# Kernel optimization log

Hardware: AMD Instinct MI355X
Metric: run time of the kernel (lower is better)

The kernel has to match this reference:

```python
import jax, jax.numpy as jnp
import numpy as np

N_NODES = 100000
N_EDGES = 3200000
FEAT = 64  # pos(32) + vel(32)
OUT_DIM = 2


def setup_inputs() -> dict:
    key = jax.random.key(0)
    k1, k2, k3, k4, k5, k6, k7, k8 = jax.random.split(key, 8)
    pos = jax.random.normal(k1, (N_NODES, 32), dtype=jnp.float32)
    vel = jax.random.normal(k2, (N_NODES, 32), dtype=jnp.float32)
    edge_index = jax.random.randint(k3, (2, N_EDGES), 0, N_NODES, dtype=jnp.int64 if jax.config.jax_enable_x64 else jnp.int32)
    s = 1.0 / np.sqrt(FEAT)
    W_rel = jax.random.uniform(k4, (FEAT, FEAT), jnp.float32, -s, s)
    b_rel = jax.random.uniform(k5, (FEAT,), jnp.float32, -s, s)
    W_root = jax.random.uniform(k6, (FEAT, FEAT), jnp.float32, -s, s)
    W_pred = jax.random.uniform(k7, (FEAT, OUT_DIM), jnp.float32, -s, s)
    b_pred = jax.random.uniform(k8, (OUT_DIM,), jnp.float32, -s, s)
    return {"pos": pos, "vel": vel, "edge_index": edge_index,
            "W_rel": W_rel, "b_rel": b_rel, "W_root": W_root,
            "W_pred": W_pred, "b_pred": b_pred}


def reference(pos, vel, edge_index, W_rel, b_rel, W_root, W_pred, b_pred):
    # h = cat([pos, vel], -1)  -> [N, 64]
    h = jnp.concatenate([pos, vel], axis=-1)
    src, dst = edge_index[0], edge_index[1]
    # GraphConv (PyG, aggr='add'): out_i = lin_rel(sum_{j->i} h_j) + lin_root(h_i)
    msgs = h[src]  # [E, 64] irregular gather
    agg = jax.ops.segment_sum(msgs, dst, num_segments=N_NODES)  # [N, 64]
    conv_out = agg @ W_rel + b_rel + h @ W_root
    # lin_pred
    return conv_out @ W_pred + b_pred
```

## Files before the change

kernel.cpp:

```cpp
#include <hip/hip_runtime.h>

#define N_NODES 100000
#define N_EDGES 3200000
#define FEAT 64
#define OUT_DIM 2

#define SHIFT 8
#define S_NODES 256
#define K_BUCKETS 391
#define CAP 8704
#define NB 400
#define EPB (N_EDGES / NB)
#define BT 1024


__global__ __launch_bounds__(256) void node_kernel(const float* __restrict__ pos,
                                                   const float* __restrict__ vel,
                                                   const float* __restrict__ W_rel,
                                                   const float* __restrict__ b_rel,
                                                   const float* __restrict__ W_root,
                                                   const float* __restrict__ W_pred,
                                                   const float* __restrict__ b_pred,
                                                   float* __restrict__ y,
                                                   float* __restrict__ out,
                                                   int* __restrict__ gcount) {
    __shared__ float sM[258];
    int t = threadIdx.x;

    if (blockIdx.x == 0)
        for (int i = t; i < K_BUCKETS; i += 256) gcount[i] = 0;

    {
        const float* W = (t < 128) ? W_rel : W_root;
        int k = (t & 127) >> 1, o = t & 1;
        float acc = 0.f;
        #pragma unroll
        for (int f = 0; f < FEAT; ++f) acc += W[k * FEAT + f] * W_pred[f * OUT_DIM + o];
        sM[t] = acc;
        if (t < OUT_DIM) {
            float b = b_pred[t];
            #pragma unroll
            for (int f = 0; f < FEAT; ++f) b += b_rel[f] * W_pred[f * OUT_DIM + t];
            sM[256 + t] = b;
        }
    }
    __syncthreads();

    int n = blockIdx.x * 256 + t;
    if (n >= N_NODES) return;

    const float4* p4 = (const float4*)(pos + (size_t)n * 32);
    const float4* v4 = (const float4*)(vel + (size_t)n * 32);
    float h[FEAT];
    #pragma unroll
    for (int i = 0; i < 8; ++i) {
        float4 a = p4[i];
        h[i * 4 + 0] = a.x; h[i * 4 + 1] = a.y; h[i * 4 + 2] = a.z; h[i * 4 + 3] = a.w;
    }
    #pragma unroll
    for (int i = 0; i < 8; ++i) {
        float4 a = v4[i];
        h[32 + i * 4 + 0] = a.x; h[32 + i * 4 + 1] = a.y; h[32 + i * 4 + 2] = a.z; h[32 + i * 4 + 3] = a.w;
    }

    float rel0 = 0.f, rel1 = 0.f, ro0 = 0.f, ro1 = 0.f;
    #pragma unroll
    for (int k = 0; k < FEAT; ++k) {
        float hk = h[k];
        rel0 += hk * sM[2 * k + 0];
        rel1 += hk * sM[2 * k + 1];
        ro0  += hk * sM[128 + 2 * k + 0];
        ro1  += hk * sM[128 + 2 * k + 1];
    }
    ((float2*)y)[n]   = make_float2(rel0, rel1);
    ((float2*)out)[n] = make_float2(ro0 + sM[256], ro1 + sM[257]);
}

__global__ __launch_bounds__(BT) void binscatter_kernel(const int* __restrict__ edges,
                                                        int* __restrict__ gcount,
                                                        unsigned* __restrict__ scat) {
    __shared__ int hist[K_BUCKETS];
    __shared__ int cum[K_BUCKETS + 1];
    __shared__ int base[K_BUCKETS];
    __shared__ int pos[K_BUCKETS];
    __shared__ unsigned sortbuf[EPB];

    int t = threadIdx.x;
    for (int i = t; i < K_BUCKETS; i += BT) hist[i] = 0;
    __syncthreads();

    const int4* s4 = (const int4*)(edges) + blockIdx.x * (EPB / 4);
    const int4* d4 = (const int4*)(edges + N_EDGES) + blockIdx.x * (EPB / 4);
    int4 sreg[2], dreg[2];
    bool valid[2];
    #pragma unroll
    for (int r = 0; r < 2; ++r) {
        int i = t + r * BT;
        valid[r] = (i < EPB / 4);
        if (valid[r]) { sreg[r] = s4[i]; dreg[r] = d4[i]; }
    }

    #pragma unroll
    for (int r = 0; r < 2; ++r) {
        if (!valid[r]) continue;
        int4 d = dreg[r];
        atomicAdd(&hist[d.x >> SHIFT], 1);
        atomicAdd(&hist[d.y >> SHIFT], 1);
        atomicAdd(&hist[d.z >> SHIFT], 1);
        atomicAdd(&hist[d.w >> SHIFT], 1);
    }
    __syncthreads();

    for (int i = t; i < K_BUCKETS; i += BT) base[i] = atomicAdd(&gcount[i], hist[i]);
    if (t < 64) {
        int lo = t * 7;
        int vals[7];
        int lsum = 0;
        #pragma unroll
        for (int j = 0; j < 7; ++j) {
            int idx = lo + j;
            int v = (idx < K_BUCKETS) ? hist[idx] : 0;
            vals[j] = lsum;
            lsum += v;
        }
        int x = lsum;
        #pragma unroll
        for (int d = 1; d < 64; d <<= 1) {
            int up = __shfl_up(x, d);
            if (t >= d) x += up;
        }
        int excl = x - lsum;
        #pragma unroll
        for (int j = 0; j < 7; ++j) {
            int idx = lo + j;
            if (idx < K_BUCKETS) { cum[idx] = excl + vals[j]; pos[idx] = excl + vals[j]; }
        }
        if (t == 63) cum[K_BUCKETS] = excl + lsum;
    }
    __syncthreads();

    #pragma unroll
    for (int r = 0; r < 2; ++r) {
        if (!valid[r]) continue;
        int4 s = sreg[r];
        int4 d = dreg[r];
        int k, p;
        k = d.x >> SHIFT; p = atomicAdd(&pos[k], 1);
        sortbuf[p] = (unsigned)s.x | ((unsigned)(d.x & (S_NODES - 1)) << 17);
        k = d.y >> SHIFT; p = atomicAdd(&pos[k], 1);
        sortbuf[p] = (unsigned)s.y | ((unsigned)(d.y & (S_NODES - 1)) << 17);
        k = d.z >> SHIFT; p = atomicAdd(&pos[k], 1);
        sortbuf[p] = (unsigned)s.z | ((unsigned)(d.z & (S_NODES - 1)) << 17);
        k = d.w >> SHIFT; p = atomicAdd(&pos[k], 1);
        sortbuf[p] = (unsigned)s.w | ((unsigned)(d.w & (S_NODES - 1)) << 17);
    }
    __syncthreads();

    int wid = t >> 6, lane = t & 63;
    for (int k = wid; k < K_BUCKETS; k += BT / 64) {
        int s0 = cum[k], s1 = cum[k + 1], b = base[k];
        for (int j = s0 + lane; j < s1; j += 64) {
            int p = b + (j - s0);
            if (p < CAP) scat[(size_t)k * CAP + p] = sortbuf[j];
        }
    }
}

__global__ __launch_bounds__(BT) void accum_kernel(const unsigned* __restrict__ scat,
                                                   const int* __restrict__ gcount,
                                                   const float* __restrict__ y,
                                                   float* __restrict__ out) {
    __shared__ float acc[S_NODES * 2];
    int t = threadIdx.x;
    if (t < S_NODES * 2) acc[t] = 0.f;
    __syncthreads();

    int k = blockIdx.x;
    int c = gcount[k];
    if (c > CAP) c = CAP;
    const unsigned* sl = scat + (size_t)k * CAP;
    const float2* y2 = (const float2*)y;
    for (int i = t; i < c; i += BT) {
        unsigned p = sl[i];
        int src = p & 0x1FFFF;
        int dl = p >> 17;
        float2 v = y2[src];
        atomicAdd(&acc[dl], v.x);
        atomicAdd(&acc[S_NODES + dl], v.y);
    }
    __syncthreads();

    if (t < S_NODES) {
        int node = k * S_NODES + t;
        if (node < N_NODES) {
            float2* o2 = (float2*)out;
            float2 cv = o2[node];
            cv.x += acc[t];
            cv.y += acc[S_NODES + t];
            o2[node] = cv;
        }
    }
}

extern "C" void kernel_launch(void* const* d_in, const int* in_sizes, int n_in,
                              void* d_out, int out_size, void* d_ws, size_t ws_size,
                              hipStream_t stream) {
    const float* pos    = (const float*)d_in[0];
    const float* vel    = (const float*)d_in[1];
    const int*   edges  = (const int*)d_in[2];
    const float* W_rel  = (const float*)d_in[3];
    const float* b_rel  = (const float*)d_in[4];
    const float* W_root = (const float*)d_in[5];
    const float* W_pred = (const float*)d_in[6];
    const float* b_pred = (const float*)d_in[7];
    float* out = (float*)d_out;

    char* ws = (char*)d_ws;
    float*    y      = (float*)(ws + 2048);
    int*      gcount = (int*)(ws + 802048);
    unsigned* scat   = (unsigned*)(ws + 803712);

    int node_blocks = (N_NODES + 255) / 256;
    node_kernel<<<node_blocks, 256, 0, stream>>>(pos, vel, W_rel, b_rel, W_root,
                                                 W_pred, b_pred, y, out, gcount);

    binscatter_kernel<<<NB, BT, 0, stream>>>(edges, gcount, scat);

    accum_kernel<<<K_BUCKETS, BT, 0, stream>>>(scat, gcount, y, out);
}
```

Measured before the change: 165.5 us.

## Partition edges by source range, stage bf16 y in LDS for accumulation

Edges are now binned by destination block of 1024 nodes and by source partition of 12500 nodes. Each accumulate block loops over the 8 source partitions, loads that slice of y into shared memory and gathers from LDS instead of doing random global reads. The per-node projected values y are packed as two bf16 in one 32-bit word, which halves the gather footprint and makes each partition fit in LDS. The cost is reduced precision of the aggregated messages, fewer accumulate blocks (98) and therefore less parallelism, and a larger histogram and scan in the scatter kernel.

```diff
diff --git a/kernel.cpp b/kernel.cpp
--- a/kernel.cpp
+++ b/kernel.cpp
@@ -5,10 +5,12 @@
 #define FEAT 64
 #define OUT_DIM 2
 
-#define SHIFT 8
-#define S_NODES 256
-#define K_BUCKETS 391
-#define CAP 8704
+#define K_DST 98
+#define DST_SZ 1024
+#define NPART 8
+#define PART_SZ 12500
+#define NSUB (K_DST * NPART)
+#define CAP_SUB 4480
 #define NB 400
 #define EPB (N_EDGES / NB)
 #define BT 1024
@@ -21,14 +23,14 @@
                                                    const float* __restrict__ W_root,
                                                    const float* __restrict__ W_pred,
                                                    const float* __restrict__ b_pred,
-                                                   float* __restrict__ y,
+                                                   unsigned* __restrict__ y,
                                                    float* __restrict__ out,
                                                    int* __restrict__ gcount) {
     __shared__ float sM[258];
     int t = threadIdx.x;
 
     if (blockIdx.x == 0)
-        for (int i = t; i < K_BUCKETS; i += 256) gcount[i] = 0;
+        for (int i = t; i < NSUB; i += 256) gcount[i] = 0;
 
     {
         const float* W = (t < 128) ? W_rel : W_root;
@@ -72,21 +74,25 @@
         ro0  += hk * sM[128 + 2 * k + 0];
         ro1  += hk * sM[128 + 2 * k + 1];
     }
-    ((float2*)y)[n]   = make_float2(rel0, rel1);
+    unsigned bx = __float_as_uint(rel0);
+    unsigned by = __float_as_uint(rel1);
+    bx += 0x7FFFu + ((bx >> 16) & 1u);
+    by += 0x7FFFu + ((by >> 16) & 1u);
+    y[n] = (bx >> 16) | (by & 0xFFFF0000u);
     ((float2*)out)[n] = make_float2(ro0 + sM[256], ro1 + sM[257]);
 }
 
 __global__ __launch_bounds__(BT) void binscatter_kernel(const int* __restrict__ edges,
                                                         int* __restrict__ gcount,
                                                         unsigned* __restrict__ scat) {
-    __shared__ int hist[K_BUCKETS];
-    __shared__ int cum[K_BUCKETS + 1];
-    __shared__ int base[K_BUCKETS];
-    __shared__ int pos[K_BUCKETS];
+    __shared__ int hist[NSUB];
+    __shared__ int cum[NSUB + 1];
+    __shared__ int base[NSUB];
+    __shared__ int rpos[NSUB];
     __shared__ unsigned sortbuf[EPB];
 
     int t = threadIdx.x;
-    for (int i = t; i < K_BUCKETS; i += BT) hist[i] = 0;
+    for (int i = t; i < NSUB; i += BT) hist[i] = 0;
     __syncthreads();
 
     const int4* s4 = (const int4*)(edges) + blockIdx.x * (EPB / 4);
@@ -103,23 +109,24 @@
     #pragma unroll
     for (int r = 0; r < 2; ++r) {
         if (!valid[r]) continue;
+        int4 s = sreg[r];
         int4 d = dreg[r];
-        atomicAdd(&hist[d.x >> SHIFT], 1);
-        atomicAdd(&hist[d.y >> SHIFT], 1);
-        atomicAdd(&hist[d.z >> SHIFT], 1);
-        atomicAdd(&hist[d.w >> SHIFT], 1);
-    }
-    __syncthreads();
-
-    for (int i = t; i < K_BUCKETS; i += BT) base[i] = atomicAdd(&gcount[i], hist[i]);
+        atomicAdd(&hist[((unsigned)d.x >> 10) * NPART + (unsigned)s.x / PART_SZ], 1);
+        atomicAdd(&hist[((unsigned)d.y >> 10) * NPART + (unsigned)s.y / PART_SZ], 1);
+        atomicAdd(&hist[((unsigned)d.z >> 10) * NPART + (unsigned)s.z / PART_SZ], 1);
+        atomicAdd(&hist[((unsigned)d.w >> 10) * NPART + (unsigned)s.w / PART_SZ], 1);
+    }
+    __syncthreads();
+
+    for (int i = t; i < NSUB; i += BT) base[i] = atomicAdd(&gcount[i], hist[i]);
     if (t < 64) {
-        int lo = t * 7;
-        int vals[7];
+        int lo = t * 13;
+        int vals[13];
         int lsum = 0;
         #pragma unroll
-        for (int j = 0; j < 7; ++j) {
+        for (int j = 0; j < 13; ++j) {
             int idx = lo + j;
-            int v = (idx < K_BUCKETS) ? hist[idx] : 0;
+            int v = (idx < NSUB) ? hist[idx] : 0;
             vals[j] = lsum;
             lsum += v;
         }
@@ -131,11 +138,11 @@
         }
         int excl = x - lsum;
         #pragma unroll
-        for (int j = 0; j < 7; ++j) {
+        for (int j = 0; j < 13; ++j) {
             int idx = lo + j;
-            if (idx < K_BUCKETS) { cum[idx] = excl + vals[j]; pos[idx] = excl + vals[j]; }
-        }
-        if (t == 63) cum[K_BUCKETS] = excl + lsum;
+            if (idx < NSUB) { cum[idx] = excl + vals[j]; rpos[idx] = excl + vals[j]; }
+        }
+        if (t == 63) cum[NSUB] = excl + lsum;
     }
     __syncthreads();
 
@@ -145,60 +152,72 @@
         int4 s = sreg[r];
         int4 d = dreg[r];
         int k, p;
-        k = d.x >> SHIFT; p = atomicAdd(&pos[k], 1);
-        sortbuf[p] = (unsigned)s.x | ((unsigned)(d.x & (S_NODES - 1)) << 17);
-        k = d.y >> SHIFT; p = atomicAdd(&pos[k], 1);
-        sortbuf[p] = (unsigned)s.y | ((unsigned)(d.y & (S_NODES - 1)) << 17);
-        k = d.z >> SHIFT; p = atomicAdd(&pos[k], 1);
-        sortbuf[p] = (unsigned)s.z | ((unsigned)(d.z & (S_NODES - 1)) << 17);
-        k = d.w >> SHIFT; p = atomicAdd(&pos[k], 1);
-        sortbuf[p] = (unsigned)s.w | ((unsigned)(d.w & (S_NODES - 1)) << 17);
+        k = ((unsigned)d.x >> 10) * NPART + (unsigned)s.x / PART_SZ;
+        p = atomicAdd(&rpos[k], 1);
+        sortbuf[p] = (unsigned)s.x | (((unsigned)d.x & (DST_SZ - 1)) << 17);
+        k = ((unsigned)d.y >> 10) * NPART + (unsigned)s.y / PART_SZ;
+        p = atomicAdd(&rpos[k], 1);
+        sortbuf[p] = (unsigned)s.y | (((unsigned)d.y & (DST_SZ - 1)) << 17);
+        k = ((unsigned)d.z >> 10) * NPART + (unsigned)s.z / PART_SZ;
+        p = atomicAdd(&rpos[k], 1);
+        sortbuf[p] = (unsigned)s.z | (((unsigned)d.z & (DST_SZ - 1)) << 17);
+        k = ((unsigned)d.w >> 10) * NPART + (unsigned)s.w / PART_SZ;
+        p = atomicAdd(&rpos[k], 1);
+        sortbuf[p] = (unsigned)s.w | (((unsigned)d.w & (DST_SZ - 1)) << 17);
     }
     __syncthreads();
 
     int wid = t >> 6, lane = t & 63;
-    for (int k = wid; k < K_BUCKETS; k += BT / 64) {
+    for (int k = wid; k < NSUB; k += BT / 64) {
         int s0 = cum[k], s1 = cum[k + 1], b = base[k];
         for (int j = s0 + lane; j < s1; j += 64) {
             int p = b + (j - s0);
-            if (p < CAP) scat[(size_t)k * CAP + p] = sortbuf[j];
+            if (p < CAP_SUB) scat[(size_t)k * CAP_SUB + p] = sortbuf[j];
         }
     }
 }
 
 __global__ __launch_bounds__(BT) void accum_kernel(const unsigned* __restrict__ scat,
                                                    const int* __restrict__ gcount,
-                                                   const float* __restrict__ y,
+                                                   const unsigned* __restrict__ y,
                                                    float* __restrict__ out) {
-    __shared__ float acc[S_NODES * 2];
+    __shared__ unsigned yl[PART_SZ];
+    __shared__ float accx[DST_SZ];
+    __shared__ float accy[DST_SZ];
+
     int t = threadIdx.x;
-    if (t < S_NODES * 2) acc[t] = 0.f;
-    __syncthreads();
-
-    int k = blockIdx.x;
-    int c = gcount[k];
-    if (c > CAP) c = CAP;
-    const unsigned* sl = scat + (size_t)k * CAP;
-    const float2* y2 = (const float2*)y;
-    for (int i = t; i < c; i += BT) {
-        unsigned p = sl[i];
-        int src = p & 0x1FFFF;
-        int dl = p >> 17;
-        float2 v = y2[src];
-        atomicAdd(&acc[dl], v.x);
-        atomicAdd(&acc[S_NODES + dl], v.y);
-    }
-    __syncthreads();
-
-    if (t < S_NODES) {
-        int node = k * S_NODES + t;
-        if (node < N_NODES) {
-            float2* o2 = (float2*)out;
-            float2 cv = o2[node];
-            cv.x += acc[t];
-            cv.y += acc[S_NODES + t];
-            o2[node] = cv;
-        }
+    int kd = blockIdx.x;
+    accx[t] = 0.f;
+    accy[t] = 0.f;
+
+    for (int p = 0; p < NPART; ++p) {
+        const unsigned* yp = y + p * PART_SZ;
+        for (int i = t; i < PART_SZ; i += BT) yl[i] = yp[i];
+        __syncthreads();
+
+        int sub = kd * NPART + p;
+        int c = gcount[sub];
+        if (c > CAP_SUB) c = CAP_SUB;
+        const unsigned* sl = scat + (size_t)sub * CAP_SUB;
+        int pbase = p * PART_SZ;
+        for (int i = t; i < c; i += BT) {
+            unsigned e = sl[i];
+            int slocal = (int)(e & 0x1FFFF) - pbase;
+            int dl = e >> 17;
+            unsigned v = yl[slocal];
+            atomicAdd(&accx[dl], __uint_as_float(v << 16));
+            atomicAdd(&accy[dl], __uint_as_float(v & 0xFFFF0000u));
+        }
+        __syncthreads();
+    }
+
+    int n = kd * DST_SZ + t;
+    if (n < N_NODES) {
+        float2* o2 = (float2*)out;
+        float2 cv = o2[n];
+        cv.x += accx[t];
+        cv.y += accy[t];
+        o2[n] = cv;
     }
 }
 
@@ -216,9 +235,9 @@
     float* out = (float*)d_out;
 
     char* ws = (char*)d_ws;
-    float*    y      = (float*)(ws + 2048);
-    int*      gcount = (int*)(ws + 802048);
-    unsigned* scat   = (unsigned*)(ws + 803712);
+    unsigned* y      = (unsigned*)(ws + 2048);
+    int*      gcount = (int*)(ws + 402048);
+    unsigned* scat   = (unsigned*)(ws + 405184);
 
     int node_blocks = (N_NODES + 255) / 256;
     node_kernel<<<node_blocks, 256, 0, stream>>>(pos, vel, W_rel, b_rel, W_root,
@@ -226,5 +245,5 @@
 
     binscatter_kernel<<<NB, BT, 0, stream>>>(edges, gcount, scat);
 
-    accum_kernel<<<K_BUCKETS, BT, 0, stream>>>(scat, gcount, y, out);
-}
+    accum_kernel<<<K_DST, BT, 0, stream>>>(scat, gcount, y, out);
+}
```

Result: slower. 240.3 us (+45.2%).
